# Kernel optimization log

Hardware: AMD Instinct MI355X
Metric: run time of the kernel (lower is better)

Reference implementation:

```python
import jax, jax.numpy as jnp
import numpy as np

N = 30000      # num nodes
E = 600000     # num edges
D = 128        # feature dim (all layers)
R = 7          # num_relation
G = 16         # num graphs in batch
L = 3          # num layers (hidden_dims = [128,128,128])


def setup_inputs() -> dict:
    key = jax.random.key(0)
    ks = jax.random.split(key, 10)
    x = jax.random.normal(ks[0], (N, D), dtype=jnp.float32)
    node_in = jax.random.randint(ks[1], (E,), 0, N)
    node_out = jax.random.randint(ks[2], (E,), 0, N)
    relation = jax.random.randint(ks[3], (E,), 0, R)
    edge_weight = jax.random.uniform(ks[4], (E,), dtype=jnp.float32)
    node2graph = jnp.sort(jax.random.randint(ks[5], (N,), 0, G))
    # learned params: per-layer relational linear (R*D -> D) and self-loop linear (D -> D)
    Wr = jax.random.normal(ks[6], (L, R * D, D), dtype=jnp.float32) * 0.02
    br = jnp.zeros((L, D), dtype=jnp.float32)
    Wl = jax.random.normal(ks[7], (L, D, D), dtype=jnp.float32) * 0.02
    bl = jnp.zeros((L, D), dtype=jnp.float32)
    return dict(x=x, node_in=node_in, node_out=node_out, relation=relation,
                edge_weight=edge_weight, node2graph=node2graph,
                Wr=Wr, br=br, Wl=Wl, bl=bl)


def reference(x, node_in, node_out, relation, edge_weight, node2graph, Wr, br, Wl, bl):
    # relation-indexed destination segment: node_out * R + relation
    seg = node_out * R + relation            # (E,)
    ew = edge_weight[:, None]                # (E, 1)
    h = x
    for i in range(L):
        msg = h[node_in] * ew                                         # gather + weight, (E, D)
        upd = jax.ops.segment_sum(msg, seg, num_segments=N * R)       # scatter_add, (N*R, D)
        upd = upd.reshape(N, R * D)                                   # per-relation concat
        h = jax.nn.relu(upd @ Wr[i] + br[i] + h @ Wl[i] + bl[i])      # linear + self-loop + act
    node_feature = h                                                  # (N, D)
    graph_feature = jax.ops.segment_sum(node_feature, node2graph, num_segments=G)  # sum readout
    return graph_feature, node_feature
```

## Files before the change

### kernel.cpp

```cpp
#include <hip/hip_runtime.h>
#include <hip/hip_bf16.h>

#define NN 30000
#define NE 600000
#define DD 128
#define RR 7
#define GG 16
#define LL 3

#define NB64 ((NN + 63) / 64)

typedef short bf16x8 __attribute__((ext_vector_type(8)));
typedef float f32x4  __attribute__((ext_vector_type(4)));

__device__ __forceinline__ unsigned short f2bf(float f) {
    unsigned u = __float_as_uint(f);
    unsigned r = (u + 0x7fffu + ((u >> 16) & 1u)) >> 16;
    return (unsigned short)r;
}
__device__ __forceinline__ float bf2f(unsigned short b) {
    return __uint_as_float(((unsigned)b) << 16);
}
__device__ __forceinline__ ushort2 pk2bf(float a, float b) {
    __hip_bfloat162 t = __float22bfloat162_rn(make_float2(a, b));
    return *(ushort2*)&t;
}

__device__ __forceinline__ void gl_lds16(const void* g, void* l) {
    __builtin_amdgcn_global_load_lds(
        (const __attribute__((address_space(1))) void*)g,
        (__attribute__((address_space(3))) void*)l, 16, 0, 0);
}

__global__ __launch_bounds__(256) void pack_weights(
    const float* __restrict__ Wl,
    const float* __restrict__ Wr,
    unsigned short* __restrict__ Bw)
{
    int t = blockIdx.x * 256 + threadIdx.x;
    if (t >= LL * 1024 * DD) return;
    int l = t >> 17;
    int rem = t & 131071;
    int n = rem >> 7;
    int k = rem & 127;
    float v;
    if (n < DD) {
        v = Wl[(size_t)l * DD * DD + k * DD + n];
    } else {
        int q = n - DD;
        v = Wr[(size_t)l * RR * DD * DD + (size_t)((q >> 7) * DD + k) * DD + (q & 127)];
    }
    Bw[(size_t)l * 1024 * DD + n * DD + k] = f2bf(v);
}

__global__ __launch_bounds__(256) void convert_bf16(
    const float* __restrict__ in, unsigned short* __restrict__ out, int n4)
{
    int i = blockIdx.x * 256 + threadIdx.x;
    if (i >= n4) return;
    float4 v = ((const float4*)in)[i];
    ushort2 lo = pk2bf(v.x, v.y);
    ushort2 hi = pk2bf(v.z, v.w);
    ((ushort4*)out)[i] = make_ushort4(lo.x, lo.y, hi.x, hi.y);
}

#define ASTR 128
__global__ __launch_bounds__(256) void gemm_mfma(
    const unsigned short* __restrict__ hb,
    const unsigned short* __restrict__ Bw,
    const float* __restrict__ br,
    const float* __restrict__ bl,
    unsigned short* __restrict__ haccb,
    unsigned short* __restrict__ Zb,
    int N)
{
    __shared__ unsigned short As[64 * ASTR];
    __shared__ unsigned short Bs[128 * ASTR];

    const int tid  = threadIdx.x;
    const int wave = tid >> 6;
    const int lane = tid & 63;
    const int quad = lane >> 4;
    const int l16  = lane & 15;
    const int row0 = blockIdx.x * 64;
    const int col0 = blockIdx.y * 128;

#pragma unroll
    for (int i = 0; i < 4; ++i) {
        int g = i * 4 + wave;
        gl_lds16(hb + (size_t)(row0 + g * 4) * DD + lane * 8,
                 As + g * 512);
    }
#pragma unroll
    for (int i = 0; i < 8; ++i) {
        int g = i * 4 + wave;
        gl_lds16(Bw + (size_t)col0 * DD + (size_t)g * 512 + lane * 8,
                 Bs + g * 512);
    }
    __syncthreads();

    f32x4 acc[4][2];
#pragma unroll
    for (int mt = 0; mt < 4; ++mt)
#pragma unroll
        for (int nt = 0; nt < 2; ++nt)
            acc[mt][nt] = (f32x4){0.f, 0.f, 0.f, 0.f};

    const unsigned short* As_l = As + l16 * ASTR;
    const unsigned short* Bs_l = Bs + (wave * 32 + l16) * ASTR;

#pragma unroll
    for (int kc = 0; kc < 4; ++kc) {
        int ko = kc * 32 + quad * 8;
        bf16x8 a0 = *(const bf16x8*)(As_l + 0 * 16 * ASTR + ko);
        bf16x8 a1 = *(const bf16x8*)(As_l + 1 * 16 * ASTR + ko);
        bf16x8 a2 = *(const bf16x8*)(As_l + 2 * 16 * ASTR + ko);
        bf16x8 a3 = *(const bf16x8*)(As_l + 3 * 16 * ASTR + ko);
        bf16x8 b0 = *(const bf16x8*)(Bs_l + 0 * 16 * ASTR + ko);
        bf16x8 b1 = *(const bf16x8*)(Bs_l + 1 * 16 * ASTR + ko);
        acc[0][0] = __builtin_amdgcn_mfma_f32_16x16x32_bf16(a0, b0, acc[0][0], 0, 0, 0);
        acc[1][0] = __builtin_amdgcn_mfma_f32_16x16x32_bf16(a1, b0, acc[1][0], 0, 0, 0);
        acc[2][0] = __builtin_amdgcn_mfma_f32_16x16x32_bf16(a2, b0, acc[2][0], 0, 0, 0);
        acc[3][0] = __builtin_amdgcn_mfma_f32_16x16x32_bf16(a3, b0, acc[3][0], 0, 0, 0);
        acc[0][1] = __builtin_amdgcn_mfma_f32_16x16x32_bf16(a0, b1, acc[0][1], 0, 0, 0);
        acc[1][1] = __builtin_amdgcn_mfma_f32_16x16x32_bf16(a1, b1, acc[1][1], 0, 0, 0);
        acc[2][1] = __builtin_amdgcn_mfma_f32_16x16x32_bf16(a2, b1, acc[2][1], 0, 0, 0);
        acc[3][1] = __builtin_amdgcn_mfma_f32_16x16x32_bf16(a3, b1, acc[3][1], 0, 0, 0);
    }

    const int ncol = wave * 32 + l16;
    if (col0 == 0) {
        float bias0 = br[ncol] + bl[ncol];
        float bias1 = br[ncol + 16] + bl[ncol + 16];
#pragma unroll
        for (int mt = 0; mt < 4; ++mt) {
#pragma unroll
            for (int reg = 0; reg < 4; ++reg) {
                int row = row0 + mt * 16 + quad * 4 + reg;
                if (row < N) {
                    ushort2 p = pk2bf(acc[mt][0][reg] + bias0,
                                      acc[mt][1][reg] + bias1);
                    haccb[(size_t)row * DD + ncol]      = p.x;
                    haccb[(size_t)row * DD + ncol + 16] = p.y;
                }
            }
        }
    } else {
        const int zc = col0 - DD + ncol;
#pragma unroll
        for (int mt = 0; mt < 4; ++mt) {
#pragma unroll
            for (int reg = 0; reg < 4; ++reg) {
                int row = row0 + mt * 16 + quad * 4 + reg;
                if (row < N) {
                    ushort2 p = pk2bf(acc[mt][0][reg], acc[mt][1][reg]);
                    Zb[(size_t)row * (RR * DD) + zc]      = p.x;
                    Zb[(size_t)row * (RR * DD) + zc + 16] = p.y;
                }
            }
        }
    }
}

__global__ __launch_bounds__(256) void bucket_hist(
    const int* __restrict__ node_out, int* __restrict__ bcnt, int E)
{
    int e = blockIdx.x * 256 + threadIdx.x;
    if (e < E) atomicAdd(&bcnt[(node_out[e] >> 6) * 16], 1);
}

__global__ __launch_bounds__(512) void bucket_scan(
    const int* __restrict__ bcnt, int* __restrict__ bstart,
    int* __restrict__ bcur, int nb)
{
    __shared__ int s[512];
    int t = threadIdx.x;
    int v = (t < nb) ? bcnt[t * 16] : 0;
    s[t] = v;
    __syncthreads();
#pragma unroll
    for (int off = 1; off < 512; off <<= 1) {
        int u = (t >= off) ? s[t - off] : 0;
        __syncthreads();
        s[t] += u;
        __syncthreads();
    }
    if (t <= nb) {
        int excl = s[t] - v;
        bstart[t] = excl;
        if (t < nb) bcur[t * 16] = excl;
    }
}

__global__ __launch_bounds__(256) void bucket_scatter(
    const int* __restrict__ node_in,
    const int* __restrict__ node_out,
    const int* __restrict__ relation,
    const float* __restrict__ ew,
    int* __restrict__ bcur,
    int2* __restrict__ tmp,
    int E)
{
    int e = blockIdx.x * 256 + threadIdx.x;
    if (e >= E) return;
    int o = node_out[e];
    int pos = atomicAdd(&bcur[(o >> 6) * 16], 1);
    tmp[pos] = make_int2(((o & 63) << 18) | (node_in[e] << 3) | relation[e],
                         __float_as_int(ew[e]));
}

__global__ __launch_bounds__(256) void bucket_sort(
    const int2* __restrict__ tmp,
    const int* __restrict__ bstart,
    int2* __restrict__ meta,
    int* __restrict__ start,
    int N)
{
    __shared__ int hist[64];
    __shared__ int scan[64];
    __shared__ int cur[64];
    const int b = blockIdx.x;
    const int t = threadIdx.x;
    const int s0 = bstart[b];
    const int s1 = bstart[b + 1];

    if (t < 64) hist[t] = 0;
    __syncthreads();
    for (int i = s0 + t; i < s1; i += 256)
        atomicAdd(&hist[((unsigned)tmp[i].x) >> 18], 1);
    __syncthreads();

    int v = (t < 64) ? hist[t] : 0;
    if (t < 64) scan[t] = v;
    __syncthreads();
#pragma unroll
    for (int off = 1; off < 64; off <<= 1) {
        int u = (t < 64 && t >= off) ? scan[t - off] : 0;
        __syncthreads();
        if (t < 64) scan[t] += u;
        __syncthreads();
    }
    if (t < 64) {
        int excl = scan[t] - v;
        cur[t] = s0 + excl;
        int node = b * 64 + t;
        if (node <= N) start[node] = s0 + excl;
    }
    __syncthreads();

    for (int i = s0 + t; i < s1; i += 256) {
        int2 m = tmp[i];
        int j = ((unsigned)m.x) >> 18;
        int pos = atomicAdd(&cur[j], 1);
        int key = m.x & 0x3ffff;
        int in = key >> 3, rel = key & 7;
        meta[pos] = make_int2((in * RR + rel) << 7, m.y);
    }
}

__global__ __launch_bounds__(256) void aggregate(
    const unsigned short* __restrict__ Zb,
    const int* __restrict__ start,
    const int2* __restrict__ meta,
    const unsigned short* __restrict__ haccb,
    float* __restrict__ out_f32,
    unsigned short* __restrict__ out_bf16,
    int N)
{
    int wid = (blockIdx.x * 256 + threadIdx.x) >> 6;
    int lane = threadIdx.x & 63;
    if (wid >= N) return;

    int e0 = start[wid];
    int e1 = start[wid + 1];

    float accx = 0.f, accy = 0.f;
    int e = e0;
    for (; e + 8 <= e1; e += 8) {
        unsigned u[8]; float wt[8];
#pragma unroll
        for (int j = 0; j < 8; ++j) {
            int2 m = meta[e + j];
            u[j] = *(const unsigned*)(Zb + m.x + lane * 2);
            wt[j] = __int_as_float(m.y);
        }
#pragma unroll
        for (int j = 0; j < 8; ++j) {
            accx = fmaf(wt[j], __uint_as_float(u[j] << 16), accx);
            accy = fmaf(wt[j], __uint_as_float(u[j] & 0xffff0000u), accy);
        }
    }
    for (; e + 2 <= e1; e += 2) {
        int2 m0 = meta[e];
        int2 m1 = meta[e + 1];
        unsigned u0 = *(const unsigned*)(Zb + m0.x + lane * 2);
        unsigned u1 = *(const unsigned*)(Zb + m1.x + lane * 2);
        float w0 = __int_as_float(m0.y), w1 = __int_as_float(m1.y);
        accx = fmaf(w0, __uint_as_float(u0 << 16), accx);
        accy = fmaf(w0, __uint_as_float(u0 & 0xffff0000u), accy);
        accx = fmaf(w1, __uint_as_float(u1 << 16), accx);
        accy = fmaf(w1, __uint_as_float(u1 & 0xffff0000u), accy);
    }
    if (e < e1) {
        int2 m = meta[e];
        unsigned u = *(const unsigned*)(Zb + m.x + lane * 2);
        float wt = __int_as_float(m.y);
        accx = fmaf(wt, __uint_as_float(u << 16), accx);
        accy = fmaf(wt, __uint_as_float(u & 0xffff0000u), accy);
    }

    unsigned bu = *(const unsigned*)(haccb + (size_t)wid * DD + lane * 2);
    float ox = fmaxf(bf2f((unsigned short)(bu & 0xffffu)) + accx, 0.f);
    float oy = fmaxf(bf2f((unsigned short)(bu >> 16)) + accy, 0.f);
    if (out_f32) {
        *(float2*)(out_f32 + (size_t)wid * DD + lane * 2) = make_float2(ox, oy);
    }
    if (out_bf16) {
        ushort2 o = pk2bf(ox, oy);
        *(ushort2*)(out_bf16 + (size_t)wid * DD + lane * 2) = o;
    }
}

__global__ __launch_bounds__(256) void graph_sum(
    const float* __restrict__ nf,
    const int* __restrict__ n2g,
    float* __restrict__ gf,
    int N)
{
    int t = blockIdx.x * 256 + threadIdx.x;
    int chunk = t >> 5;
    int lane = t & 31;
    int n0 = chunk * 16;
    if (n0 >= N) return;
    int nend = n0 + 16; if (nend > N) nend = N;

    float4 acc = make_float4(0.f, 0.f, 0.f, 0.f);
    int curg = n2g[n0];
    for (int n = n0; n < nend; ++n) {
        int g = n2g[n];
        if (g != curg) {
            float* dst = gf + (size_t)curg * DD + lane * 4;
            atomicAdd(dst + 0, acc.x); atomicAdd(dst + 1, acc.y);
            atomicAdd(dst + 2, acc.z); atomicAdd(dst + 3, acc.w);
            acc = make_float4(0.f, 0.f, 0.f, 0.f);
            curg = g;
        }
        float4 v = *(const float4*)(nf + (size_t)n * DD + lane * 4);
        acc.x += v.x; acc.y += v.y; acc.z += v.z; acc.w += v.w;
    }
    float* dst = gf + (size_t)curg * DD + lane * 4;
    atomicAdd(dst + 0, acc.x); atomicAdd(dst + 1, acc.y);
    atomicAdd(dst + 2, acc.z); atomicAdd(dst + 3, acc.w);
}

extern "C" void kernel_launch(void* const* d_in, const int* in_sizes, int n_in,
                              void* d_out, int out_size, void* d_ws, size_t ws_size,
                              hipStream_t stream)
{
    const float* x        = (const float*)d_in[0];
    const int*   node_in  = (const int*)d_in[1];
    const int*   node_out = (const int*)d_in[2];
    const int*   relation = (const int*)d_in[3];
    const float* ew       = (const float*)d_in[4];
    const int*   n2g      = (const int*)d_in[5];
    const float* Wr       = (const float*)d_in[6];
    const float* br       = (const float*)d_in[7];
    const float* Wl       = (const float*)d_in[8];
    const float* bl       = (const float*)d_in[9];

    float* out = (float*)d_out;
    float* gf = out;
    float* nf = out + GG * DD;

    char* w = (char*)d_ws;
    unsigned short* Zb   = (unsigned short*)w; w += (size_t)NN * RR * DD * 2;
    unsigned short* haccb= (unsigned short*)w; w += (size_t)NN * DD * 2;
    unsigned short* hbA  = (unsigned short*)w; w += (size_t)NN * DD * 2;
    unsigned short* hbB  = (unsigned short*)w; w += (size_t)NN * DD * 2;
    unsigned short* Bw   = (unsigned short*)w; w += (size_t)LL * 1024 * DD * 2;
    int2*  meta   = (int2*)w;                  w += (size_t)NE * 8;
    int2*  tmp    = (int2*)w;                  w += (size_t)NE * 8;
    int*   start  = (int*)w;                   w += (size_t)(NN + 1) * 4 + 60;
    int*   bcnt   = (int*)w;                   w += (size_t)NB64 * 16 * 4 + 64;
    int*   bcur   = (int*)w;                   w += (size_t)NB64 * 16 * 4 + 64;
    int*   bstart = (int*)w;                   w += (size_t)(NB64 + 1) * 4 + 60;

    const int N = NN, E = NE;

    pack_weights<<<(LL * 1024 * DD + 255) / 256, 256, 0, stream>>>(Wl, Wr, Bw);
    convert_bf16<<<(N * DD / 4 + 255) / 256, 256, 0, stream>>>(x, hbA, N * DD / 4);

    hipMemsetAsync(bcnt, 0, (size_t)NB64 * 16 * sizeof(int), stream);
    bucket_hist<<<(E + 255) / 256, 256, 0, stream>>>(node_out, bcnt, E);
    bucket_scan<<<1, 512, 0, stream>>>(bcnt, bstart, bcur, NB64);
    bucket_scatter<<<(E + 255) / 256, 256, 0, stream>>>(
        node_in, node_out, relation, ew, bcur, tmp, E);
    bucket_sort<<<NB64, 256, 0, stream>>>(tmp, bstart, meta, start, N);

    dim3 ggrid((N + 63) / 64, 8);
    unsigned short* hin = hbA;
    unsigned short* hnext = hbB;
    for (int l = 0; l < LL; ++l) {
        const float* br_l = br + (size_t)l * DD;
        const float* bl_l = bl + (size_t)l * DD;
        const unsigned short* Bw_l = Bw + (size_t)l * 1024 * DD;

        gemm_mfma<<<ggrid, 256, 0, stream>>>(hin, Bw_l, br_l, bl_l, haccb, Zb, N);

        bool last = (l == LL - 1);
        aggregate<<<(N * 64 + 255) / 256, 256, 0, stream>>>(
            Zb, start, meta, haccb,
            last ? nf : (float*)nullptr,
            last ? (unsigned short*)nullptr : hnext, N);

        unsigned short* t = hin; hin = hnext; hnext = t;
    }

    hipMemsetAsync(gf, 0, (size_t)GG * DD * sizeof(float), stream);
    int chunks = (N + 15) / 16;
    graph_sum<<<(chunks * 32 + 255) / 256, 256, 0, stream>>>(nf, n2g, gf, N);
}
```

Measured before the change: 344.5 us.

## Aggregate raw features per relation before a single fused K=1024 GEMM

The order of operations is reversed. The old code ran the GEMM first to produce per-relation transformed features Z (N×7×128) and then gathered rows of Z along edges. The new code gathers rows of h (128 wide) per edge, accumulates them into 7 per-relation register accumulators, and writes a bf16 upd buffer. One GEMM over K=1024 (self-loop plus 7 relations) then applies bias and ReLU, using an XOR-swizzled LDS layout. Edge gathers now touch a much smaller working set, and the GEMM grid shrinks from 8 column tiles to 1. The cost is an extra bf16 write and read of upd and a per-edge relation switch. The GEMM now loops over 8 K-chunks with synchronisation and has less block parallelism.

```diff
diff --git a/kernel.cpp b/kernel.cpp
--- a/kernel.cpp
+++ b/kernel.cpp
@@ -35,22 +35,22 @@
 __global__ __launch_bounds__(256) void pack_weights(
     const float* __restrict__ Wl,
     const float* __restrict__ Wr,
-    unsigned short* __restrict__ Bw)
+    unsigned short* __restrict__ Bw2)
 {
     int t = blockIdx.x * 256 + threadIdx.x;
-    if (t >= LL * 1024 * DD) return;
-    int l = t >> 17;
-    int rem = t & 131071;
-    int n = rem >> 7;
-    int k = rem & 127;
+    if (t >= LL * 131072) return;
+    int l    = t >> 17;
+    int rem  = t & 131071;
+    int ch   = rem >> 14;
+    int c    = (rem >> 7) & 127;
+    int kkin = rem & 127;
     float v;
-    if (n < DD) {
-        v = Wl[(size_t)l * DD * DD + k * DD + n];
+    if (ch == 0) {
+        v = Wl[(size_t)l * 16384 + kkin * 128 + c];
     } else {
-        int q = n - DD;
-        v = Wr[(size_t)l * RR * DD * DD + (size_t)((q >> 7) * DD + k) * DD + (q & 127)];
-    }
-    Bw[(size_t)l * 1024 * DD + n * DD + k] = f2bf(v);
+        v = Wr[(size_t)l * 114688 + (size_t)((ch - 1) * 128 + kkin) * 128 + c];
+    }
+    Bw2[t] = f2bf(v);
 }
 
 __global__ __launch_bounds__(256) void convert_bf16(
@@ -62,104 +62,6 @@
     ushort2 lo = pk2bf(v.x, v.y);
     ushort2 hi = pk2bf(v.z, v.w);
     ((ushort4*)out)[i] = make_ushort4(lo.x, lo.y, hi.x, hi.y);
-}
-
-#define ASTR 128
-__global__ __launch_bounds__(256) void gemm_mfma(
-    const unsigned short* __restrict__ hb,
-    const unsigned short* __restrict__ Bw,
-    const float* __restrict__ br,
-    const float* __restrict__ bl,
-    unsigned short* __restrict__ haccb,
-    unsigned short* __restrict__ Zb,
-    int N)
-{
-    __shared__ unsigned short As[64 * ASTR];
-    __shared__ unsigned short Bs[128 * ASTR];
-
-    const int tid  = threadIdx.x;
-    const int wave = tid >> 6;
-    const int lane = tid & 63;
-    const int quad = lane >> 4;
-    const int l16  = lane & 15;
-    const int row0 = blockIdx.x * 64;
-    const int col0 = blockIdx.y * 128;
-
-#pragma unroll
-    for (int i = 0; i < 4; ++i) {
-        int g = i * 4 + wave;
-        gl_lds16(hb + (size_t)(row0 + g * 4) * DD + lane * 8,
-                 As + g * 512);
-    }
-#pragma unroll
-    for (int i = 0; i < 8; ++i) {
-        int g = i * 4 + wave;
-        gl_lds16(Bw + (size_t)col0 * DD + (size_t)g * 512 + lane * 8,
-                 Bs + g * 512);
-    }
-    __syncthreads();
-
-    f32x4 acc[4][2];
-#pragma unroll
-    for (int mt = 0; mt < 4; ++mt)
-#pragma unroll
-        for (int nt = 0; nt < 2; ++nt)
-            acc[mt][nt] = (f32x4){0.f, 0.f, 0.f, 0.f};
-
-    const unsigned short* As_l = As + l16 * ASTR;
-    const unsigned short* Bs_l = Bs + (wave * 32 + l16) * ASTR;
-
-#pragma unroll
-    for (int kc = 0; kc < 4; ++kc) {
-        int ko = kc * 32 + quad * 8;
-        bf16x8 a0 = *(const bf16x8*)(As_l + 0 * 16 * ASTR + ko);
-        bf16x8 a1 = *(const bf16x8*)(As_l + 1 * 16 * ASTR + ko);
-        bf16x8 a2 = *(const bf16x8*)(As_l + 2 * 16 * ASTR + ko);
-        bf16x8 a3 = *(const bf16x8*)(As_l + 3 * 16 * ASTR + ko);
-        bf16x8 b0 = *(const bf16x8*)(Bs_l + 0 * 16 * ASTR + ko);
-        bf16x8 b1 = *(const bf16x8*)(Bs_l + 1 * 16 * ASTR + ko);
-        acc[0][0] = __builtin_amdgcn_mfma_f32_16x16x32_bf16(a0, b0, acc[0][0], 0, 0, 0);
-        acc[1][0] = __builtin_amdgcn_mfma_f32_16x16x32_bf16(a1, b0, acc[1][0], 0, 0, 0);
-        acc[2][0] = __builtin_amdgcn_mfma_f32_16x16x32_bf16(a2, b0, acc[2][0], 0, 0, 0);
-        acc[3][0] = __builtin_amdgcn_mfma_f32_16x16x32_bf16(a3, b0, acc[3][0], 0, 0, 0);
-        acc[0][1] = __builtin_amdgcn_mfma_f32_16x16x32_bf16(a0, b1, acc[0][1], 0, 0, 0);
-        acc[1][1] = __builtin_amdgcn_mfma_f32_16x16x32_bf16(a1, b1, acc[1][1], 0, 0, 0);
-        acc[2][1] = __builtin_amdgcn_mfma_f32_16x16x32_bf16(a2, b1, acc[2][1], 0, 0, 0);
-        acc[3][1] = __builtin_amdgcn_mfma_f32_16x16x32_bf16(a3, b1, acc[3][1], 0, 0, 0);
-    }
-
-    const int ncol = wave * 32 + l16;
-    if (col0 == 0) {
-        float bias0 = br[ncol] + bl[ncol];
-        float bias1 = br[ncol + 16] + bl[ncol + 16];
-#pragma unroll
-        for (int mt = 0; mt < 4; ++mt) {
-#pragma unroll
-            for (int reg = 0; reg < 4; ++reg) {
-                int row = row0 + mt * 16 + quad * 4 + reg;
-                if (row < N) {
-                    ushort2 p = pk2bf(acc[mt][0][reg] + bias0,
-                                      acc[mt][1][reg] + bias1);
-                    haccb[(size_t)row * DD + ncol]      = p.x;
-                    haccb[(size_t)row * DD + ncol + 16] = p.y;
-                }
-            }
-        }
-    } else {
-        const int zc = col0 - DD + ncol;
-#pragma unroll
-        for (int mt = 0; mt < 4; ++mt) {
-#pragma unroll
-            for (int reg = 0; reg < 4; ++reg) {
-                int row = row0 + mt * 16 + quad * 4 + reg;
-                if (row < N) {
-                    ushort2 p = pk2bf(acc[mt][0][reg], acc[mt][1][reg]);
-                    Zb[(size_t)row * (RR * DD) + zc]      = p.x;
-                    Zb[(size_t)row * (RR * DD) + zc + 16] = p.y;
-                }
-            }
-        }
-    }
 }
 
 __global__ __launch_bounds__(256) void bucket_hist(
@@ -252,19 +154,15 @@
         int2 m = tmp[i];
         int j = ((unsigned)m.x) >> 18;
         int pos = atomicAdd(&cur[j], 1);
-        int key = m.x & 0x3ffff;
-        int in = key >> 3, rel = key & 7;
-        meta[pos] = make_int2((in * RR + rel) << 7, m.y);
-    }
-}
-
-__global__ __launch_bounds__(256) void aggregate(
-    const unsigned short* __restrict__ Zb,
+        meta[pos] = make_int2(m.x & 0x3ffff, m.y);
+    }
+}
+
+__global__ __launch_bounds__(256) void aggregate_h(
+    const unsigned short* __restrict__ hb,
     const int* __restrict__ start,
     const int2* __restrict__ meta,
-    const unsigned short* __restrict__ haccb,
-    float* __restrict__ out_f32,
-    unsigned short* __restrict__ out_bf16,
+    unsigned short* __restrict__ upd,
     int N)
 {
     int wid = (blockIdx.x * 256 + threadIdx.x) >> 6;
@@ -274,50 +172,149 @@
     int e0 = start[wid];
     int e1 = start[wid + 1];
 
-    float accx = 0.f, accy = 0.f;
+    float ax[7], ay[7];
+#pragma unroll
+    for (int r = 0; r < 7; ++r) { ax[r] = 0.f; ay[r] = 0.f; }
+
+#define GATHER(m) (*(const unsigned*)(hb + (((size_t)((m).x >> 3)) << 7) + lane * 2))
+#define ACCUM(m, u) do {                                                       \
+    float w_  = __int_as_float((m).y);                                         \
+    float hx_ = __uint_as_float((u) << 16);                                    \
+    float hy_ = __uint_as_float((u) & 0xffff0000u);                            \
+    switch (__builtin_amdgcn_readfirstlane((m).x) & 7) {                       \
+      case 0: ax[0]=fmaf(w_,hx_,ax[0]); ay[0]=fmaf(w_,hy_,ay[0]); break;       \
+      case 1: ax[1]=fmaf(w_,hx_,ax[1]); ay[1]=fmaf(w_,hy_,ay[1]); break;       \
+      case 2: ax[2]=fmaf(w_,hx_,ax[2]); ay[2]=fmaf(w_,hy_,ay[2]); break;       \
+      case 3: ax[3]=fmaf(w_,hx_,ax[3]); ay[3]=fmaf(w_,hy_,ay[3]); break;       \
+      case 4: ax[4]=fmaf(w_,hx_,ax[4]); ay[4]=fmaf(w_,hy_,ay[4]); break;       \
+      case 5: ax[5]=fmaf(w_,hx_,ax[5]); ay[5]=fmaf(w_,hy_,ay[5]); break;       \
+      default: ax[6]=fmaf(w_,hx_,ax[6]); ay[6]=fmaf(w_,hy_,ay[6]); break;      \
+    } } while (0)
+
     int e = e0;
-    for (; e + 8 <= e1; e += 8) {
-        unsigned u[8]; float wt[8];
-#pragma unroll
-        for (int j = 0; j < 8; ++j) {
-            int2 m = meta[e + j];
-            u[j] = *(const unsigned*)(Zb + m.x + lane * 2);
-            wt[j] = __int_as_float(m.y);
+    for (; e + 4 <= e1; e += 4) {
+        int2 m0 = meta[e + 0], m1 = meta[e + 1];
+        int2 m2 = meta[e + 2], m3 = meta[e + 3];
+        unsigned u0 = GATHER(m0), u1 = GATHER(m1);
+        unsigned u2 = GATHER(m2), u3 = GATHER(m3);
+        ACCUM(m0, u0); ACCUM(m1, u1); ACCUM(m2, u2); ACCUM(m3, u3);
+    }
+    for (; e < e1; ++e) {
+        int2 m = meta[e];
+        unsigned u = GATHER(m);
+        ACCUM(m, u);
+    }
+#undef GATHER
+#undef ACCUM
+
+    unsigned short* urow = upd + (size_t)wid * 896 + lane * 2;
+#pragma unroll
+    for (int r = 0; r < 7; ++r) {
+        ushort2 p = pk2bf(ax[r], ay[r]);
+        *(unsigned*)(urow + r * 128) = ((unsigned)p.y << 16) | p.x;
+    }
+}
+
+__global__ __launch_bounds__(256) void gemm_fused(
+    const unsigned short* __restrict__ hb,
+    const unsigned short* __restrict__ upd,
+    const unsigned short* __restrict__ Bw2,
+    const float* __restrict__ br,
+    const float* __restrict__ bl,
+    unsigned short* __restrict__ hout,
+    float* __restrict__ nf,
+    int N)
+{
+    __shared__ unsigned short As[64 * 128];
+    __shared__ unsigned short Bs[128 * 128];
+
+    const int tid  = threadIdx.x;
+    const int wave = tid >> 6;
+    const int lane = tid & 63;
+    const int quad = lane >> 4;
+    const int l16  = lane & 15;
+    const int row0 = blockIdx.x * 64;
+
+    const int lr = lane >> 4;
+    const int ls = lane & 15;
+
+    f32x4 acc[4][2];
+#pragma unroll
+    for (int mt = 0; mt < 4; ++mt)
+#pragma unroll
+        for (int nt = 0; nt < 2; ++nt)
+            acc[mt][nt] = (f32x4){0.f, 0.f, 0.f, 0.f};
+
+    const unsigned short* As_l = As + l16 * 128;
+    const unsigned short* Bs_l = Bs + (wave * 32 + l16) * 128;
+    const int swz = l16 & 7;
+
+    for (int ch = 0; ch < 8; ++ch) {
+#pragma unroll
+        for (int i = 0; i < 4; ++i) {
+            int g = i * 4 + wave;
+            int r = g * 4 + lr;
+            int slot = ls ^ (r & 7);
+            const unsigned short* src;
+            if (ch == 0)
+                src = hb + (size_t)(row0 + r) * 128 + slot * 8;
+            else
+                src = upd + (size_t)(row0 + r) * 896 + (ch - 1) * 128 + slot * 8;
+            gl_lds16(src, As + g * 512);
         }
-#pragma unroll
-        for (int j = 0; j < 8; ++j) {
-            accx = fmaf(wt[j], __uint_as_float(u[j] << 16), accx);
-            accy = fmaf(wt[j], __uint_as_float(u[j] & 0xffff0000u), accy);
+        const unsigned short* Bchunk = Bw2 + (size_t)ch * 16384;
+#pragma unroll
+        for (int i = 0; i < 8; ++i) {
+            int g = i * 4 + wave;
+            int r = g * 4 + lr;
+            int slot = ls ^ (r & 7);
+            gl_lds16(Bchunk + (size_t)r * 128 + slot * 8, Bs + g * 512);
         }
-    }
-    for (; e + 2 <= e1; e += 2) {
-        int2 m0 = meta[e];
-        int2 m1 = meta[e + 1];
-        unsigned u0 = *(const unsigned*)(Zb + m0.x + lane * 2);
-        unsigned u1 = *(const unsigned*)(Zb + m1.x + lane * 2);
-        float w0 = __int_as_float(m0.y), w1 = __int_as_float(m1.y);
-        accx = fmaf(w0, __uint_as_float(u0 << 16), accx);
-        accy = fmaf(w0, __uint_as_float(u0 & 0xffff0000u), accy);
-        accx = fmaf(w1, __uint_as_float(u1 << 16), accx);
-        accy = fmaf(w1, __uint_as_float(u1 & 0xffff0000u), accy);
-    }
-    if (e < e1) {
-        int2 m = meta[e];
-        unsigned u = *(const unsigned*)(Zb + m.x + lane * 2);
-        float wt = __int_as_float(m.y);
-        accx = fmaf(wt, __uint_as_float(u << 16), accx);
-        accy = fmaf(wt, __uint_as_float(u & 0xffff0000u), accy);
-    }
-
-    unsigned bu = *(const unsigned*)(haccb + (size_t)wid * DD + lane * 2);
-    float ox = fmaxf(bf2f((unsigned short)(bu & 0xffffu)) + accx, 0.f);
-    float oy = fmaxf(bf2f((unsigned short)(bu >> 16)) + accy, 0.f);
-    if (out_f32) {
-        *(float2*)(out_f32 + (size_t)wid * DD + lane * 2) = make_float2(ox, oy);
-    }
-    if (out_bf16) {
-        ushort2 o = pk2bf(ox, oy);
-        *(ushort2*)(out_bf16 + (size_t)wid * DD + lane * 2) = o;
+        __syncthreads();
+
+#pragma unroll
+        for (int kc = 0; kc < 4; ++kc) {
+            int so = ((kc * 4 + quad) ^ swz) * 8;
+            bf16x8 a0 = *(const bf16x8*)(As_l + 0 * 16 * 128 + so);
+            bf16x8 a1 = *(const bf16x8*)(As_l + 1 * 16 * 128 + so);
+            bf16x8 a2 = *(const bf16x8*)(As_l + 2 * 16 * 128 + so);
+            bf16x8 a3 = *(const bf16x8*)(As_l + 3 * 16 * 128 + so);
+            bf16x8 b0 = *(const bf16x8*)(Bs_l + 0 * 16 * 128 + so);
+            bf16x8 b1 = *(const bf16x8*)(Bs_l + 1 * 16 * 128 + so);
+            acc[0][0] = __builtin_amdgcn_mfma_f32_16x16x32_bf16(a0, b0, acc[0][0], 0, 0, 0);
+            acc[1][0] = __builtin_amdgcn_mfma_f32_16x16x32_bf16(a1, b0, acc[1][0], 0, 0, 0);
+            acc[2][0] = __builtin_amdgcn_mfma_f32_16x16x32_bf16(a2, b0, acc[2][0], 0, 0, 0);
+            acc[3][0] = __builtin_amdgcn_mfma_f32_16x16x32_bf16(a3, b0, acc[3][0], 0, 0, 0);
+            acc[0][1] = __builtin_amdgcn_mfma_f32_16x16x32_bf16(a0, b1, acc[0][1], 0, 0, 0);
+            acc[1][1] = __builtin_amdgcn_mfma_f32_16x16x32_bf16(a1, b1, acc[1][1], 0, 0, 0);
+            acc[2][1] = __builtin_amdgcn_mfma_f32_16x16x32_bf16(a2, b1, acc[2][1], 0, 0, 0);
+            acc[3][1] = __builtin_amdgcn_mfma_f32_16x16x32_bf16(a3, b1, acc[3][1], 0, 0, 0);
+        }
+        __syncthreads();
+    }
+
+    const int ncol = wave * 32 + l16;
+    float bias0 = br[ncol] + bl[ncol];
+    float bias1 = br[ncol + 16] + bl[ncol + 16];
+#pragma unroll
+    for (int mt = 0; mt < 4; ++mt) {
+#pragma unroll
+        for (int reg = 0; reg < 4; ++reg) {
+            int row = row0 + mt * 16 + quad * 4 + reg;
+            if (row < N) {
+                float v0 = fmaxf(acc[mt][0][reg] + bias0, 0.f);
+                float v1 = fmaxf(acc[mt][1][reg] + bias1, 0.f);
+                if (hout) {
+                    ushort2 p = pk2bf(v0, v1);
+                    hout[(size_t)row * DD + ncol]      = p.x;
+                    hout[(size_t)row * DD + ncol + 16] = p.y;
+                }
+                if (nf) {
+                    nf[(size_t)row * DD + ncol]      = v0;
+                    nf[(size_t)row * DD + ncol + 16] = v1;
+                }
+            }
+        }
     }
 }
 
@@ -373,11 +370,10 @@
     float* nf = out + GG * DD;
 
     char* w = (char*)d_ws;
-    unsigned short* Zb   = (unsigned short*)w; w += (size_t)NN * RR * DD * 2;
-    unsigned short* haccb= (unsigned short*)w; w += (size_t)NN * DD * 2;
+    unsigned short* upd  = (unsigned short*)w; w += (size_t)NN * RR * DD * 2;
     unsigned short* hbA  = (unsigned short*)w; w += (size_t)NN * DD * 2;
     unsigned short* hbB  = (unsigned short*)w; w += (size_t)NN * DD * 2;
-    unsigned short* Bw   = (unsigned short*)w; w += (size_t)LL * 1024 * DD * 2;
+    unsigned short* Bw2  = (unsigned short*)w; w += (size_t)LL * 131072 * 2;
     int2*  meta   = (int2*)w;                  w += (size_t)NE * 8;
     int2*  tmp    = (int2*)w;                  w += (size_t)NE * 8;
     int*   start  = (int*)w;                   w += (size_t)(NN + 1) * 4 + 60;
@@ -387,7 +383,7 @@
 
     const int N = NN, E = NE;
 
-    pack_weights<<<(LL * 1024 * DD + 255) / 256, 256, 0, stream>>>(Wl, Wr, Bw);
+    pack_weights<<<(LL * 131072 + 255) / 256, 256, 0, stream>>>(Wl, Wr, Bw2);
     convert_bf16<<<(N * DD / 4 + 255) / 256, 256, 0, stream>>>(x, hbA, N * DD / 4);
 
     hipMemsetAsync(bcnt, 0, (size_t)NB64 * 16 * sizeof(int), stream);
@@ -397,21 +393,21 @@
         node_in, node_out, relation, ew, bcur, tmp, E);
     bucket_sort<<<NB64, 256, 0, stream>>>(tmp, bstart, meta, start, N);
 
-    dim3 ggrid((N + 63) / 64, 8);
     unsigned short* hin = hbA;
     unsigned short* hnext = hbB;
     for (int l = 0; l < LL; ++l) {
         const float* br_l = br + (size_t)l * DD;
         const float* bl_l = bl + (size_t)l * DD;
-        const unsigned short* Bw_l = Bw + (size_t)l * 1024 * DD;
-
-        gemm_mfma<<<ggrid, 256, 0, stream>>>(hin, Bw_l, br_l, bl_l, haccb, Zb, N);
-
+        const unsigned short* Bw2_l = Bw2 + (size_t)l * 131072;
         bool last = (l == LL - 1);
-        aggregate<<<(N * 64 + 255) / 256, 256, 0, stream>>>(
-            Zb, start, meta, haccb,
-            last ? nf : (float*)nullptr,
-            last ? (unsigned short*)nullptr : hnext, N);
+
+        aggregate_h<<<(N * 64 + 255) / 256, 256, 0, stream>>>(
+            hin, start, meta, upd, N);
+
+        gemm_fused<<<(N + 63) / 64, 256, 0, stream>>>(
+            hin, upd, Bw2_l, br_l, bl_l,
+            last ? (unsigned short*)nullptr : hnext,
+            last ? nf : (float*)nullptr, N);
 
         unsigned short* t = hin; hin = hnext; hnext = t;
     }
```

New measurement: 358.1 us. +3.9%, slower.

## Widen GEMM tile to 256 columns and XOR-swizzle LDS layout

Applied to the files above, without the earlier changes.

The MFMA GEMM now computes a 64x256 output tile per block (4x4 accumulators per wave) instead of 64x128, halving the grid's column dimension so each A tile load is reused across twice as many output columns. LDS rows are stored with an XOR swizzle on 16-byte slots to avoid bank conflicts on the unpadded 128-element stride. Bucket-sort kernels are only moved earlier in the file. The larger B tile raises LDS use to 80KB per block and doubles accumulator registers, which may reduce occupancy.

```diff
diff --git a/kernel.cpp b/kernel.cpp
--- a/kernel.cpp
+++ b/kernel.cpp
@@ -64,7 +64,102 @@
     ((ushort4*)out)[i] = make_ushort4(lo.x, lo.y, hi.x, hi.y);
 }
 
-#define ASTR 128
+__global__ __launch_bounds__(256) void bucket_hist(
+    const int* __restrict__ node_out, int* __restrict__ bcnt, int E)
+{
+    int e = blockIdx.x * 256 + threadIdx.x;
+    if (e < E) atomicAdd(&bcnt[(node_out[e] >> 6) * 16], 1);
+}
+
+__global__ __launch_bounds__(512) void bucket_scan(
+    const int* __restrict__ bcnt, int* __restrict__ bstart,
+    int* __restrict__ bcur, int nb)
+{
+    __shared__ int s[512];
+    int t = threadIdx.x;
+    int v = (t < nb) ? bcnt[t * 16] : 0;
+    s[t] = v;
+    __syncthreads();
+#pragma unroll
+    for (int off = 1; off < 512; off <<= 1) {
+        int u = (t >= off) ? s[t - off] : 0;
+        __syncthreads();
+        s[t] += u;
+        __syncthreads();
+    }
+    if (t <= nb) {
+        int excl = s[t] - v;
+        bstart[t] = excl;
+        if (t < nb) bcur[t * 16] = excl;
+    }
+}
+
+__global__ __launch_bounds__(256) void bucket_scatter(
+    const int* __restrict__ node_in,
+    const int* __restrict__ node_out,
+    const int* __restrict__ relation,
+    const float* __restrict__ ew,
+    int* __restrict__ bcur,
+    int2* __restrict__ tmp,
+    int E)
+{
+    int e = blockIdx.x * 256 + threadIdx.x;
+    if (e >= E) return;
+    int o = node_out[e];
+    int pos = atomicAdd(&bcur[(o >> 6) * 16], 1);
+    tmp[pos] = make_int2(((o & 63) << 18) | (node_in[e] << 3) | relation[e],
+                         __float_as_int(ew[e]));
+}
+
+__global__ __launch_bounds__(256) void bucket_sort(
+    const int2* __restrict__ tmp,
+    const int* __restrict__ bstart,
+    int2* __restrict__ meta,
+    int* __restrict__ start,
+    int N)
+{
+    __shared__ int hist[64];
+    __shared__ int scan[64];
+    __shared__ int cur[64];
+    const int b = blockIdx.x;
+    const int t = threadIdx.x;
+    const int s0 = bstart[b];
+    const int s1 = bstart[b + 1];
+
+    if (t < 64) hist[t] = 0;
+    __syncthreads();
+    for (int i = s0 + t; i < s1; i += 256)
+        atomicAdd(&hist[((unsigned)tmp[i].x) >> 18], 1);
+    __syncthreads();
+
+    int v = (t < 64) ? hist[t] : 0;
+    if (t < 64) scan[t] = v;
+    __syncthreads();
+#pragma unroll
+    for (int off = 1; off < 64; off <<= 1) {
+        int u = (t < 64 && t >= off) ? scan[t - off] : 0;
+        __syncthreads();
+        if (t < 64) scan[t] += u;
+        __syncthreads();
+    }
+    if (t < 64) {
+        int excl = scan[t] - v;
+        cur[t] = s0 + excl;
+        int node = b * 64 + t;
+        if (node <= N) start[node] = s0 + excl;
+    }
+    __syncthreads();
+
+    for (int i = s0 + t; i < s1; i += 256) {
+        int2 m = tmp[i];
+        int j = ((unsigned)m.x) >> 18;
+        int pos = atomicAdd(&cur[j], 1);
+        int key = m.x & 0x3ffff;
+        int in = key >> 3, rel = key & 7;
+        meta[pos] = make_int2((in * RR + rel) << 7, m.y);
+    }
+}
+
 __global__ __launch_bounds__(256) void gemm_mfma(
     const unsigned short* __restrict__ hb,
     const unsigned short* __restrict__ Bw,
@@ -74,8 +169,8 @@
     unsigned short* __restrict__ Zb,
     int N)
 {
-    __shared__ unsigned short As[64 * ASTR];
-    __shared__ unsigned short Bs[128 * ASTR];
+    __shared__ unsigned short As[64 * 128];
+    __shared__ unsigned short Bs[256 * 128];
 
     const int tid  = threadIdx.x;
     const int wave = tid >> 6;
@@ -83,178 +178,102 @@
     const int quad = lane >> 4;
     const int l16  = lane & 15;
     const int row0 = blockIdx.x * 64;
-    const int col0 = blockIdx.y * 128;
+    const int col0 = blockIdx.y * 256;
+
+    const int lr = lane >> 4;
+    const int ls = lane & 15;
 
 #pragma unroll
     for (int i = 0; i < 4; ++i) {
         int g = i * 4 + wave;
-        gl_lds16(hb + (size_t)(row0 + g * 4) * DD + lane * 8,
-                 As + g * 512);
-    }
-#pragma unroll
-    for (int i = 0; i < 8; ++i) {
+        int r = g * 4 + lr;
+        int slot = ls ^ (r & 7);
+        gl_lds16(hb + (size_t)(row0 + r) * 128 + slot * 8, As + g * 512);
+    }
+#pragma unroll
+    for (int i = 0; i < 16; ++i) {
         int g = i * 4 + wave;
-        gl_lds16(Bw + (size_t)col0 * DD + (size_t)g * 512 + lane * 8,
-                 Bs + g * 512);
-    }
-    __syncthreads();
-
-    f32x4 acc[4][2];
+        int r = g * 4 + lr;
+        int slot = ls ^ (r & 7);
+        gl_lds16(Bw + (size_t)(col0 + r) * 128 + slot * 8, Bs + g * 512);
+    }
+    __syncthreads();
+
+    f32x4 acc[4][4];
 #pragma unroll
     for (int mt = 0; mt < 4; ++mt)
 #pragma unroll
-        for (int nt = 0; nt < 2; ++nt)
+        for (int nt = 0; nt < 4; ++nt)
             acc[mt][nt] = (f32x4){0.f, 0.f, 0.f, 0.f};
 
-    const unsigned short* As_l = As + l16 * ASTR;
-    const unsigned short* Bs_l = Bs + (wave * 32 + l16) * ASTR;
+    const unsigned short* As_l = As + l16 * 128;
+    const unsigned short* Bs_l = Bs + (wave * 64 + l16) * 128;
+    const int swz = l16 & 7;
 
 #pragma unroll
     for (int kc = 0; kc < 4; ++kc) {
-        int ko = kc * 32 + quad * 8;
-        bf16x8 a0 = *(const bf16x8*)(As_l + 0 * 16 * ASTR + ko);
-        bf16x8 a1 = *(const bf16x8*)(As_l + 1 * 16 * ASTR + ko);
-        bf16x8 a2 = *(const bf16x8*)(As_l + 2 * 16 * ASTR + ko);
-        bf16x8 a3 = *(const bf16x8*)(As_l + 3 * 16 * ASTR + ko);
-        bf16x8 b0 = *(const bf16x8*)(Bs_l + 0 * 16 * ASTR + ko);
-        bf16x8 b1 = *(const bf16x8*)(Bs_l + 1 * 16 * ASTR + ko);
-        acc[0][0] = __builtin_amdgcn_mfma_f32_16x16x32_bf16(a0, b0, acc[0][0], 0, 0, 0);
-        acc[1][0] = __builtin_amdgcn_mfma_f32_16x16x32_bf16(a1, b0, acc[1][0], 0, 0, 0);
-        acc[2][0] = __builtin_amdgcn_mfma_f32_16x16x32_bf16(a2, b0, acc[2][0], 0, 0, 0);
-        acc[3][0] = __builtin_amdgcn_mfma_f32_16x16x32_bf16(a3, b0, acc[3][0], 0, 0, 0);
-        acc[0][1] = __builtin_amdgcn_mfma_f32_16x16x32_bf16(a0, b1, acc[0][1], 0, 0, 0);
-        acc[1][1] = __builtin_amdgcn_mfma_f32_16x16x32_bf16(a1, b1, acc[1][1], 0, 0, 0);
-        acc[2][1] = __builtin_amdgcn_mfma_f32_16x16x32_bf16(a2, b1, acc[2][1], 0, 0, 0);
-        acc[3][1] = __builtin_amdgcn_mfma_f32_16x16x32_bf16(a3, b1, acc[3][1], 0, 0, 0);
-    }
-
-    const int ncol = wave * 32 + l16;
-    if (col0 == 0) {
-        float bias0 = br[ncol] + bl[ncol];
-        float bias1 = br[ncol + 16] + bl[ncol + 16];
+        int so = ((kc * 4 + quad) ^ swz) * 8;
+        bf16x8 a0 = *(const bf16x8*)(As_l + 0 * 16 * 128 + so);
+        bf16x8 a1 = *(const bf16x8*)(As_l + 1 * 16 * 128 + so);
+        bf16x8 a2 = *(const bf16x8*)(As_l + 2 * 16 * 128 + so);
+        bf16x8 a3 = *(const bf16x8*)(As_l + 3 * 16 * 128 + so);
+        bf16x8 b0 = *(const bf16x8*)(Bs_l + 0 * 16 * 128 + so);
+        bf16x8 b1 = *(const bf16x8*)(Bs_l + 1 * 16 * 128 + so);
+        bf16x8 b2 = *(const bf16x8*)(Bs_l + 2 * 16 * 128 + so);
+        bf16x8 b3 = *(const bf16x8*)(Bs_l + 3 * 16 * 128 + so);
+#pragma unroll
+        for (int mt = 0; mt < 4; ++mt) {
+            bf16x8 a = (mt == 0) ? a0 : (mt == 1) ? a1 : (mt == 2) ? a2 : a3;
+            acc[mt][0] = __builtin_amdgcn_mfma_f32_16x16x32_bf16(a, b0, acc[mt][0], 0, 0, 0);
+            acc[mt][1] = __builtin_amdgcn_mfma_f32_16x16x32_bf16(a, b1, acc[mt][1], 0, 0, 0);
+            acc[mt][2] = __builtin_amdgcn_mfma_f32_16x16x32_bf16(a, b2, acc[mt][2], 0, 0, 0);
+            acc[mt][3] = __builtin_amdgcn_mfma_f32_16x16x32_bf16(a, b3, acc[mt][3], 0, 0, 0);
+        }
+    }
+
+    if (col0 == 0 && wave < 2) {
+        float bias[4];
+#pragma unroll
+        for (int nt = 0; nt < 4; ++nt) {
+            int c = wave * 64 + nt * 16 + l16;
+            bias[nt] = br[c] + bl[c];
+        }
 #pragma unroll
         for (int mt = 0; mt < 4; ++mt) {
 #pragma unroll
             for (int reg = 0; reg < 4; ++reg) {
                 int row = row0 + mt * 16 + quad * 4 + reg;
                 if (row < N) {
-                    ushort2 p = pk2bf(acc[mt][0][reg] + bias0,
-                                      acc[mt][1][reg] + bias1);
-                    haccb[(size_t)row * DD + ncol]      = p.x;
-                    haccb[(size_t)row * DD + ncol + 16] = p.y;
+                    ushort2 p01 = pk2bf(acc[mt][0][reg] + bias[0],
+                                        acc[mt][1][reg] + bias[1]);
+                    ushort2 p23 = pk2bf(acc[mt][2][reg] + bias[2],
+                                        acc[mt][3][reg] + bias[3]);
+                    unsigned short* dst = haccb + (size_t)row * 128 + wave * 64 + l16;
+                    dst[0]  = p01.x;
+                    dst[16] = p01.y;
+                    dst[32] = p23.x;
+                    dst[48] = p23.y;
                 }
             }
         }
     } else {
-        const int zc = col0 - DD + ncol;
+        const int zc = col0 + wave * 64 - 128;
 #pragma unroll
         for (int mt = 0; mt < 4; ++mt) {
 #pragma unroll
             for (int reg = 0; reg < 4; ++reg) {
                 int row = row0 + mt * 16 + quad * 4 + reg;
                 if (row < N) {
-                    ushort2 p = pk2bf(acc[mt][0][reg], acc[mt][1][reg]);
-                    Zb[(size_t)row * (RR * DD) + zc]      = p.x;
-                    Zb[(size_t)row * (RR * DD) + zc + 16] = p.y;
+                    ushort2 p01 = pk2bf(acc[mt][0][reg], acc[mt][1][reg]);
+                    ushort2 p23 = pk2bf(acc[mt][2][reg], acc[mt][3][reg]);
+                    unsigned short* dst = Zb + (size_t)row * (RR * DD) + zc + l16;
+                    dst[0]  = p01.x;
+                    dst[16] = p01.y;
+                    dst[32] = p23.x;
+                    dst[48] = p23.y;
                 }
             }
         }
-    }
-}
-
-__global__ __launch_bounds__(256) void bucket_hist(
-    const int* __restrict__ node_out, int* __restrict__ bcnt, int E)
-{
-    int e = blockIdx.x * 256 + threadIdx.x;
-    if (e < E) atomicAdd(&bcnt[(node_out[e] >> 6) * 16], 1);
-}
-
-__global__ __launch_bounds__(512) void bucket_scan(
-    const int* __restrict__ bcnt, int* __restrict__ bstart,
-    int* __restrict__ bcur, int nb)
-{
-    __shared__ int s[512];
-    int t = threadIdx.x;
-    int v = (t < nb) ? bcnt[t * 16] : 0;
-    s[t] = v;
-    __syncthreads();
-#pragma unroll
-    for (int off = 1; off < 512; off <<= 1) {
-        int u = (t >= off) ? s[t - off] : 0;
-        __syncthreads();
-        s[t] += u;
-        __syncthreads();
-    }
-    if (t <= nb) {
-        int excl = s[t] - v;
-        bstart[t] = excl;
-        if (t < nb) bcur[t * 16] = excl;
-    }
-}
-
-__global__ __launch_bounds__(256) void bucket_scatter(
-    const int* __restrict__ node_in,
-    const int* __restrict__ node_out,
-    const int* __restrict__ relation,
-    const float* __restrict__ ew,
-    int* __restrict__ bcur,
-    int2* __restrict__ tmp,
-    int E)
-{
-    int e = blockIdx.x * 256 + threadIdx.x;
-    if (e >= E) return;
-    int o = node_out[e];
-    int pos = atomicAdd(&bcur[(o >> 6) * 16], 1);
-    tmp[pos] = make_int2(((o & 63) << 18) | (node_in[e] << 3) | relation[e],
-                         __float_as_int(ew[e]));
-}
-
-__global__ __launch_bounds__(256) void bucket_sort(
-    const int2* __restrict__ tmp,
-    const int* __restrict__ bstart,
-    int2* __restrict__ meta,
-    int* __restrict__ start,
-    int N)
-{
-    __shared__ int hist[64];
-    __shared__ int scan[64];
-    __shared__ int cur[64];
-    const int b = blockIdx.x;
-    const int t = threadIdx.x;
-    const int s0 = bstart[b];
-    const int s1 = bstart[b + 1];
-
-    if (t < 64) hist[t] = 0;
-    __syncthreads();
-    for (int i = s0 + t; i < s1; i += 256)
-        atomicAdd(&hist[((unsigned)tmp[i].x) >> 18], 1);
-    __syncthreads();
-
-    int v = (t < 64) ? hist[t] : 0;
-    if (t < 64) scan[t] = v;
-    __syncthreads();
-#pragma unroll
-    for (int off = 1; off < 64; off <<= 1) {
-        int u = (t < 64 && t >= off) ? scan[t - off] : 0;
-        __syncthreads();
-        if (t < 64) scan[t] += u;
-        __syncthreads();
-    }
-    if (t < 64) {
-        int excl = scan[t] - v;
-        cur[t] = s0 + excl;
-        int node = b * 64 + t;
-        if (node <= N) start[node] = s0 + excl;
-    }
-    __syncthreads();
-
-    for (int i = s0 + t; i < s1; i += 256) {
-        int2 m = tmp[i];
-        int j = ((unsigned)m.x) >> 18;
-        int pos = atomicAdd(&cur[j], 1);
-        int key = m.x & 0x3ffff;
-        int in = key >> 3, rel = key & 7;
-        meta[pos] = make_int2((in * RR + rel) << 7, m.y);
     }
 }
 
@@ -397,7 +416,7 @@
         node_in, node_out, relation, ew, bcur, tmp, E);
     bucket_sort<<<NB64, 256, 0, stream>>>(tmp, bstart, meta, start, N);
 
-    dim3 ggrid((N + 63) / 64, 8);
+    dim3 ggrid((N + 63) / 64, 4);
     unsigned short* hin = hbA;
     unsigned short* hnext = hbB;
     for (int l = 0; l < LL; ++l) {
```

Measured after the change: 329.5 us. 1.05x faster.
